# Performance work log

Hardware: AMD Instinct MI355X
Metric: run time of the kernel (lower is better)

The kernel has to match this reference:

```python
import jax, jax.numpy as jnp
import numpy as np
from jax import lax

N, L, D = 8, 2048, 512
KS = [3, 5]
DECAY = 0.2


def setup_inputs() -> dict:
    key = jax.random.key(0)
    k1, k2, k3, k4, k5 = jax.random.split(key, 5)
    return {
        "qa_embed_data": jax.random.normal(k1, (N, L, D), dtype=jnp.float32),
        "conv_w3": jax.random.normal(k2, (D, 1, KS[0]), dtype=jnp.float32) * (1.0 / KS[0]),
        "conv_w5": jax.random.normal(k3, (D, 1, KS[1]), dtype=jnp.float32) * (1.0 / KS[1]),
        "fusion_w": jax.random.normal(k4, (D, 2 * D), dtype=jnp.float32) * 0.02,
        "fusion_b": jax.random.normal(k5, (D,), dtype=jnp.float32) * 0.02,
    }


def causal_depthwise_conv(x, w, k):
    # x: [N, L, C], w: [C, 1, k] (depthwise, groups=C). Left-pad by k-1 (causal).
    xc = jnp.transpose(x, (0, 2, 1))  # [N, C, L]
    y = lax.conv_general_dilated(
        xc, w, window_strides=(1,), padding=[(k - 1, 0)],
        feature_group_count=x.shape[-1],
        dimension_numbers=("NCH", "OIH", "NCH"))
    return jnp.transpose(y, (0, 2, 1))  # [N, L, C]


def squash(v):
    norm = jnp.linalg.norm(v, axis=-1, keepdims=True)
    scale = norm ** 2 / (1.0 + norm ** 2)
    return scale * v / (norm + 1e-9)


def dynamic_routing(u, num_iterations):
    # u: [N, L, M, C]
    n, l, m, _ = u.shape
    logits = jnp.zeros((n, l, m), dtype=u.dtype)
    v = None
    for i in range(num_iterations):
        c = jax.nn.softmax(logits, axis=-1)
        s = jnp.einsum("nlm,nlmc->nlc", c, u)
        v = squash(s)
        if i < num_iterations - 1:
            logits = logits + jnp.einsum("nlmc,nlc->nlm", u, v)
    return v


def time_attention(x):
    # x: [N, L, C]; causal attention with exp(-decay*dist) bias -> add -decay*dist in log space
    l = x.shape[1]
    sim = jnp.einsum("nlc,nmc->nlm", x, x)  # [N, L, L]
    idx = jnp.arange(l)
    dist = (idx[:, None] - idx[None, :]).astype(x.dtype)  # query - key
    mask = dist >= 0  # lower-triangular causal mask
    ws = jnp.where(mask[None], sim - DECAY * dist[None], -jnp.inf)
    attn = jax.nn.softmax(ws, axis=-1)
    return jnp.einsum("nlm,nmc->nlc", attn, x)


def reference(qa_embed_data, conv_w3, conv_w5, fusion_w, fusion_b):
    trend3 = causal_depthwise_conv(qa_embed_data, conv_w3, KS[0])
    trend5 = causal_depthwise_conv(qa_embed_data, conv_w5, KS[1])
    seasonal = jnp.stack([qa_embed_data - trend3, qa_embed_data - trend5], axis=2)  # [N,L,2,C]
    trend = jnp.stack([trend3, trend5], axis=2)  # [N,L,2,C]
    seasonal_f = time_attention(dynamic_routing(seasonal, 3))
    trend_f = time_attention(dynamic_routing(trend, 3))
    cat = jnp.concatenate([seasonal_f, trend_f], axis=-1)  # [N,L,2C]
    return cat @ fusion_w.T + fusion_b
```

## Files before the change

### kernel.cpp

```cpp
#include <hip/hip_runtime.h>


typedef short     bf16x8 __attribute__((ext_vector_type(8)));
typedef float     f32x4  __attribute__((ext_vector_type(4)));
typedef unsigned short u16;
typedef u16       u16x8  __attribute__((ext_vector_type(8)));
typedef u16       u16x4  __attribute__((ext_vector_type(4)));

#define NBATCH 8
#define LSEQ   2048
#define DCH    512
#define DPAD   520
#define VSTR   40
#define DECAYF 0.2f
#define WTILES 4

typedef const __attribute__((address_space(1))) unsigned char* gas_t;
typedef __attribute__((address_space(3))) unsigned char* las_t;
__device__ __forceinline__ void dma16(const void* g, void* l) {
    __builtin_amdgcn_global_load_lds((gas_t)g, (las_t)l, 16, 0, 0);
}

__device__ __forceinline__ u16 f2bf(float f) {
    unsigned int u = __float_as_uint(f);
    u += 0x7fffu + ((u >> 16) & 1u);
    return (u16)(u >> 16);
}

__device__ __forceinline__ void wave_sum6(float& a, float& b, float& c,
                                          float& d, float& e, float& f) {
#pragma unroll
    for (int m = 1; m < 64; m <<= 1) {
        float ta = __shfl_xor(a, m, 64);
        float tb = __shfl_xor(b, m, 64);
        float tc = __shfl_xor(c, m, 64);
        float td = __shfl_xor(d, m, 64);
        float te = __shfl_xor(e, m, 64);
        float tf = __shfl_xor(f, m, 64);
        a += ta; b += tb; c += tc; d += td; e += te; f += tf;
    }
}

__global__ __launch_bounds__(256) void conv_route(
    const float* __restrict__ x, const float* __restrict__ w3, const float* __restrict__ w5,
    u16* __restrict__ vs, u16* __restrict__ vt)
{
    const int wid  = threadIdx.x >> 6;
    const int lane = threadIdx.x & 63;
    const int pp   = wid >> 1;
    const int half = wid & 1;
    const int p = blockIdx.x * 2 + pp;
    const int n = p >> 11, l = p & (LSEQ - 1);
    const int c0 = half * 256 + lane * 4;

    float xm[5][4];
#pragma unroll
    for (int j = 0; j < 5; ++j) {
        int ll = l - j;
        if (ll >= 0) {
            float4 a = *(const float4*)(x + ((size_t)(n*LSEQ + ll))*DCH + c0);
            xm[j][0]=a.x; xm[j][1]=a.y; xm[j][2]=a.z; xm[j][3]=a.w;
        } else {
#pragma unroll
            for (int i = 0; i < 4; ++i) xm[j][i] = 0.f;
        }
    }
    float f3[12], f5[20];
#pragma unroll
    for (int k = 0; k < 3; ++k) ((float4*)f3)[k] = ((const float4*)(w3 + (size_t)c0*3))[k];
#pragma unroll
    for (int k = 0; k < 5; ++k) ((float4*)f5)[k] = ((const float4*)(w5 + (size_t)c0*5))[k];

    float t3[4], t5[4], a0[4], a1[4];
#pragma unroll
    for (int i = 0; i < 4; ++i) {
        t3[i] = f3[i*3+0]*xm[2][i] + f3[i*3+1]*xm[1][i] + f3[i*3+2]*xm[0][i];
        t5[i] = f5[i*5+0]*xm[4][i] + f5[i*5+1]*xm[3][i] + f5[i*5+2]*xm[2][i]
              + f5[i*5+3]*xm[1][i] + f5[i*5+4]*xm[0][i];
        a0[i] = xm[0][i] - t3[i];
        a1[i] = xm[0][i] - t5[i];
    }

    float A1=0.f, B1=0.f, C1=0.f, A2=0.f, B2=0.f, C2=0.f;
#pragma unroll
    for (int i = 0; i < 4; ++i) {
        A1 += a0[i]*a0[i]; B1 += a0[i]*a1[i]; C1 += a1[i]*a1[i];
        A2 += t3[i]*t3[i]; B2 += t3[i]*t5[i]; C2 += t5[i]*t5[i];
    }
    wave_sum6(A1, B1, C1, A2, B2, C2);

    __shared__ float red[2][2][6];
    if (lane == 0) {
        red[pp][half][0] = A1; red[pp][half][1] = B1; red[pp][half][2] = C1;
        red[pp][half][3] = A2; red[pp][half][4] = B2; red[pp][half][5] = C2;
    }
    __syncthreads();
    A1 = red[pp][0][0] + red[pp][1][0];
    B1 = red[pp][0][1] + red[pp][1][1];
    C1 = red[pp][0][2] + red[pp][1][2];
    A2 = red[pp][0][3] + red[pp][1][3];
    B2 = red[pp][0][4] + red[pp][1][4];
    C2 = red[pp][0][5] + red[pp][1][5];

    float ba0=0.f, ba1=0.f, bb0=0.f, bb1=0.f;
    float ca0=0.5f, ca1=0.5f, sca=0.f, cb0=0.5f, cb1=0.5f, scb=0.f;
#pragma unroll
    for (int it = 0; it < 3; ++it) {
        float mxa = fmaxf(ba0, ba1), mxb = fmaxf(bb0, bb1);
        float ea0 = __expf(ba0-mxa), ea1 = __expf(ba1-mxa);
        float eb0 = __expf(bb0-mxb), eb1 = __expf(bb1-mxb);
        float ia = 1.f/(ea0+ea1), ib = 1.f/(eb0+eb1);
        ca0 = ea0*ia; ca1 = ea1*ia; cb0 = eb0*ib; cb1 = eb1*ib;
        float na = ca0*ca0*A1 + 2.f*ca0*ca1*B1 + ca1*ca1*C1;
        float nb = cb0*cb0*A2 + 2.f*cb0*cb1*B2 + cb1*cb1*C2;
        sca = na / ((1.f + na) * (sqrtf(na) + 1e-9f));
        scb = nb / ((1.f + nb) * (sqrtf(nb) + 1e-9f));
        if (it < 2) {
            ba0 += sca*(ca0*A1 + ca1*B1);
            ba1 += sca*(ca0*B1 + ca1*C1);
            bb0 += scb*(cb0*A2 + cb1*B2);
            bb1 += scb*(cb0*B2 + cb1*C2);
        }
    }
    u16x4 pa, pb;
#pragma unroll
    for (int i = 0; i < 4; ++i) {
        pa[i] = f2bf(sca*(ca0*a0[i] + ca1*a1[i]));
        pb[i] = f2bf(scb*(cb0*t3[i] + cb1*t5[i]));
    }
    *(u16x4*)(vs + (size_t)p*DPAD + c0) = pa;
    *(u16x4*)(vt + (size_t)p*DPAD + c0) = pb;
}

__global__ __launch_bounds__(256) void attn(
    const u16* __restrict__ vs, const u16* __restrict__ vt,
    u16* __restrict__ cat)
{
    __shared__ u16 Ks[33792/2];
    __shared__ u16 Vs[DCH*VSTR];
    __shared__ unsigned int Ps32[4][16][20];

    const int inst = blockIdx.y;
    const int t = inst >> 3, n = inst & 7;
    const u16* src = (t ? vt : vs) + (size_t)n * LSEQ * DPAD;

    const int bx = blockIdx.x;
    const int r0 = (((bx & 7) << 2) | (bx >> 3)) * 64;

    const int tid  = threadIdx.x;
    const int wid  = tid >> 6, lane = tid & 63;
    const int l16  = lane & 15, quad = lane >> 4;

    bf16x8 qf[16];
    {
        const u16* qp = src + (size_t)(r0 + wid*16 + l16) * DPAD + quad*8;
#pragma unroll
        for (int kc = 0; kc < 16; ++kc) qf[kc] = *(const bf16x8*)(qp + kc*32);
    }

    f32x4 O[32];
#pragma unroll
    for (int i = 0; i < 32; ++i) O[i] = (f32x4){0.f, 0.f, 0.f, 0.f};
    f32x4 O2 = {0.f, 0.f, 0.f, 0.f};

    bf16x8 ones8;
#pragma unroll
    for (int i = 0; i < 8; ++i) ones8[i] = (short)0x3F80;

    const int kb_hi = (r0 >> 5) + 1;
    const int kb_lo = (kb_hi >= WTILES) ? kb_hi - (WTILES-1) : 0;

    {
        const u16* gK = src + (size_t)kb_lo * 32 * DPAD;
        for (int i = wid; i < 33; i += 4) dma16(gK + i*512 + lane*8, Ks + i*512);
    }

    for (int kb = kb_lo; kb <= kb_hi; ++kb) {
        __syncthreads();

        f32x4 S0a = {0.f,0.f,0.f,0.f}, S1a = {0.f,0.f,0.f,0.f};
        f32x4 S0b = {0.f,0.f,0.f,0.f}, S1b = {0.f,0.f,0.f,0.f};
#pragma unroll
        for (int kc = 0; kc < 8; ++kc) {
            bf16x8 b0 = *(const bf16x8*)(Ks + (size_t)l16*DPAD + kc*32 + quad*8);
            bf16x8 b1 = *(const bf16x8*)(Ks + (size_t)(16+l16)*DPAD + kc*32 + quad*8);
            S0a = __builtin_amdgcn_mfma_f32_16x16x32_bf16(qf[kc], b0, S0a, 0, 0, 0);
            S1a = __builtin_amdgcn_mfma_f32_16x16x32_bf16(qf[kc], b1, S1a, 0, 0, 0);
        }
#pragma unroll
        for (int kc = 8; kc < 16; ++kc) {
            bf16x8 b0 = *(const bf16x8*)(Ks + (size_t)l16*DPAD + kc*32 + quad*8);
            bf16x8 b1 = *(const bf16x8*)(Ks + (size_t)(16+l16)*DPAD + kc*32 + quad*8);
            S0b = __builtin_amdgcn_mfma_f32_16x16x32_bf16(qf[kc], b0, S0b, 0, 0, 0);
            S1b = __builtin_amdgcn_mfma_f32_16x16x32_bf16(qf[kc], b1, S1b, 0, 0, 0);
        }
        f32x4 S0 = S0a + S0b, S1 = S1a + S1b;

#pragma unroll
        for (int pass = 0; pass < 2; ++pass) {
            const int ch = pass*256 + tid;
#pragma unroll
            for (int g = 0; g < 4; ++g) {
                u16x8 o;
#pragma unroll
                for (int j = 0; j < 4; ++j) {
                    o[2*j]   = Ks[(size_t)(g*4 + j)      * DPAD + ch];
                    o[2*j+1] = Ks[(size_t)(g*4 + j + 16) * DPAD + ch];
                }
                *(u16x8*)(Vs + ch*VSTR + g*8) = o;
            }
        }

        const int rowg = r0 + wid*16 + quad*4;
#pragma unroll
        for (int r = 0; r < 4; ++r) {
            int row = rowg + r;
            int d0  = row - (kb*32 + l16);
            int d1  = d0 - 16;
            float p0 = (d0 >= 0) ? __expf(fmaf(-DECAYF, (float)d0, S0[r] - 1.f)) : 0.f;
            float p1 = (d1 >= 0) ? __expf(fmaf(-DECAYF, (float)d1, S1[r] - 1.f)) : 0.f;
            Ps32[wid][quad*4 + r][l16] = ((unsigned)f2bf(p1) << 16) | (unsigned)f2bf(p0);
        }

        __syncthreads();
        if (kb < kb_hi) {
            const u16* gK = src + (size_t)(kb+1) * 32 * DPAD;
            for (int i = wid; i < 33; i += 4) dma16(gK + i*512 + lane*8, Ks + i*512);
        }

        bf16x8 pf = *(const bf16x8*)(&Ps32[wid][l16][quad*4]);
#pragma unroll
        for (int ct = 0; ct < 32; ++ct) {
            bf16x8 vf = *(const bf16x8*)(Vs + (size_t)(ct*16 + l16)*VSTR + quad*8);
            O[ct] = __builtin_amdgcn_mfma_f32_16x16x32_bf16(pf, vf, O[ct], 0, 0, 0);
        }
        O2 = __builtin_amdgcn_mfma_f32_16x16x32_bf16(pf, ones8, O2, 0, 0, 0);
    }

    float inv[4];
#pragma unroll
    for (int r = 0; r < 4; ++r) inv[r] = 1.f / O2[r];
    const size_t rowbase = (size_t)n * LSEQ + r0 + wid*16 + quad*4;
    const int colbase = t * 512 + l16;
#pragma unroll
    for (int ct = 0; ct < 32; ++ct) {
#pragma unroll
        for (int r = 0; r < 4; ++r)
            cat[(rowbase + r) * 1024 + colbase + ct*16] = f2bf(O[ct][r] * inv[r]);
    }
}

__global__ __launch_bounds__(256) void cast_w(const float* __restrict__ w, u16* __restrict__ wb)
{
    int id = blockIdx.x * 256 + threadIdx.x;
    float4 f = ((const float4*)w)[id];
    u16x4 o;
    o[0] = f2bf(f.x); o[1] = f2bf(f.y); o[2] = f2bf(f.z); o[3] = f2bf(f.w);
    ((u16x4*)wb)[id] = o;
}

__global__ __launch_bounds__(256) void fusion_gemm(
    const u16* __restrict__ A, const u16* __restrict__ Wb,
    const float* __restrict__ bias, float* __restrict__ out)
{
    __shared__ u16 As[2][64*64];
    __shared__ u16 Bs[2][128*64];
    const int m0 = blockIdx.x * 64;
    const int n0 = blockIdx.y * 128;
    const int tid = threadIdx.x;
    const int wid = tid >> 6, lane = tid & 63;
    const int l16 = lane & 15, quad = lane >> 4;

    f32x4 acc[4][2];
#pragma unroll
    for (int i = 0; i < 4; ++i)
#pragma unroll
        for (int j = 0; j < 2; ++j) acc[i][j] = (f32x4){0.f, 0.f, 0.f, 0.f};

    auto stage = [&](int kb_, int b_) {
#pragma unroll
        for (int i = 0; i < 2; ++i) {
            int q = i*256 + tid, r = q >> 3, kp = q & 7;
            int kl = kp ^ (r & 7);
            dma16(A + (size_t)(m0 + r)*1024 + kb_*64 + kl*8, As[b_] + q*8);
        }
#pragma unroll
        for (int i = 0; i < 4; ++i) {
            int q = i*256 + tid, r = q >> 3, kp = q & 7;
            int kl = kp ^ (r & 7);
            dma16(Wb + (size_t)(n0 + r)*1024 + kb_*64 + kl*8, Bs[b_] + q*8);
        }
    };

    stage(0, 0);
    for (int kb = 0; kb < 16; ++kb) {
        const int b = kb & 1;
        asm volatile("s_waitcnt vmcnt(0)" ::: "memory");
        __builtin_amdgcn_s_barrier();
        asm volatile("" ::: "memory");
        if (kb < 15) stage(kb + 1, b ^ 1);
#pragma unroll
        for (int k2 = 0; k2 < 2; ++k2) {
            const int kl = k2*4 + quad;
            bf16x8 af[4], bf2[2];
#pragma unroll
            for (int i = 0; i < 4; ++i) {
                int r = i*16 + l16;
                af[i] = *(const bf16x8*)(As[b] + r*64 + (kl ^ (r & 7))*8);
            }
#pragma unroll
            for (int j = 0; j < 2; ++j) {
                int r = wid*32 + j*16 + l16;
                bf2[j] = *(const bf16x8*)(Bs[b] + r*64 + (kl ^ (r & 7))*8);
            }
#pragma unroll
            for (int i = 0; i < 4; ++i)
#pragma unroll
                for (int j = 0; j < 2; ++j)
                    acc[i][j] = __builtin_amdgcn_mfma_f32_16x16x32_bf16(af[i], bf2[j], acc[i][j], 0, 0, 0);
        }
    }
#pragma unroll
    for (int j = 0; j < 2; ++j) {
        int col = n0 + wid*32 + j*16 + l16;
        float bv = bias[col];
#pragma unroll
        for (int i = 0; i < 4; ++i) {
            int rowb = m0 + i*16 + quad*4;
#pragma unroll
            for (int r = 0; r < 4; ++r)
                out[(size_t)(rowb + r)*512 + col] = acc[i][j][r] + bv;
        }
    }
}

extern "C" void kernel_launch(void* const* d_in, const int* in_sizes, int n_in,
                              void* d_out, int out_size, void* d_ws, size_t ws_size,
                              hipStream_t stream)
{
    (void)in_sizes; (void)n_in; (void)out_size; (void)ws_size;
    const float* x  = (const float*)d_in[0];
    const float* w3 = (const float*)d_in[1];
    const float* w5 = (const float*)d_in[2];
    const float* fw = (const float*)d_in[3];
    const float* fb = (const float*)d_in[4];
    float* out = (float*)d_out;

    const size_t SZP = (size_t)NBATCH * LSEQ * DPAD;
    u16* vs   = (u16*)d_ws;
    u16* vt   = vs   + SZP;
    u16* cat  = vt   + SZP;
    u16* wb   = cat  + (size_t)NBATCH*LSEQ*1024;

    cast_w     <<<512, 256, 0, stream>>>(fw, wb);
    conv_route <<<8192, 256, 0, stream>>>(x, w3, w5, vs, vt);
    attn       <<<dim3(32, 16), 256, 0, stream>>>(vs, vt, cat);
    fusion_gemm<<<dim3(256, 4), 256, 0, stream>>>(cat, wb, fb, out);
}
```

Before: 183.8 us.

## Double-buffer K tiles in attention and triple-buffer fusion GEMM loads

The attention kernel now keeps two K tile buffers in shared memory and prefetches two tiles ahead, waiting with vmcnt counters instead of a full __syncthreads, so global loads overlap the QK/PV compute. The V transpose loop reads 32-bit pairs and writes two channels per thread instead of separate 16-bit loads. The fusion GEMM moves from a double to a triple buffer with a prefetch distance of two. This raises LDS use per block, which may lower occupancy, and the padded extra DMA slots load redundant data.

Result: faster. 177.3 us (-3.5%).

```diff
diff --git a/kernel.cpp b/kernel.cpp
--- a/kernel.cpp
+++ b/kernel.cpp
@@ -6,6 +6,8 @@
 typedef unsigned short u16;
 typedef u16       u16x8  __attribute__((ext_vector_type(8)));
 typedef u16       u16x4  __attribute__((ext_vector_type(4)));
+typedef unsigned int u32;
+typedef u32       u32x4  __attribute__((ext_vector_type(4)));
 
 #define NBATCH 8
 #define LSEQ   2048
@@ -136,7 +138,7 @@
     const u16* __restrict__ vs, const u16* __restrict__ vt,
     u16* __restrict__ cat)
 {
-    __shared__ u16 Ks[33792/2];
+    __shared__ u16 KsB[2][18432];
     __shared__ u16 Vs[DCH*VSTR];
     __shared__ unsigned int Ps32[4][16][20];
 
@@ -170,44 +172,58 @@
     const int kb_hi = (r0 >> 5) + 1;
     const int kb_lo = (kb_hi >= WTILES) ? kb_hi - (WTILES-1) : 0;
 
-    {
-        const u16* gK = src + (size_t)kb_lo * 32 * DPAD;
-        for (int i = wid; i < 33; i += 4) dma16(gK + i*512 + lane*8, Ks + i*512);
-    }
+    auto stageK = [&](int kbt, int buf) {
+        const u16* gK = src + (size_t)kbt * 32 * DPAD;
+#pragma unroll
+        for (int j = 0; j < 9; ++j) {
+            int i = wid + 4*j;
+            int is = (i < 33) ? i : 0;
+            dma16(gK + is*512 + lane*8, KsB[buf] + i*512);
+        }
+    };
+
+    stageK(kb_lo,     0);
+    stageK(kb_lo + 1, 1);
 
     for (int kb = kb_lo; kb <= kb_hi; ++kb) {
-        __syncthreads();
+        if (kb < kb_hi) asm volatile("s_waitcnt vmcnt(9)" ::: "memory");
+        else            asm volatile("s_waitcnt vmcnt(0)" ::: "memory");
+        __builtin_amdgcn_s_barrier();
+        asm volatile("" ::: "memory");
+        const u16* K = KsB[(kb - kb_lo) & 1];
 
         f32x4 S0a = {0.f,0.f,0.f,0.f}, S1a = {0.f,0.f,0.f,0.f};
         f32x4 S0b = {0.f,0.f,0.f,0.f}, S1b = {0.f,0.f,0.f,0.f};
 #pragma unroll
         for (int kc = 0; kc < 8; ++kc) {
-            bf16x8 b0 = *(const bf16x8*)(Ks + (size_t)l16*DPAD + kc*32 + quad*8);
-            bf16x8 b1 = *(const bf16x8*)(Ks + (size_t)(16+l16)*DPAD + kc*32 + quad*8);
+            bf16x8 b0 = *(const bf16x8*)(K + (size_t)l16*DPAD + kc*32 + quad*8);
+            bf16x8 b1 = *(const bf16x8*)(K + (size_t)(16+l16)*DPAD + kc*32 + quad*8);
             S0a = __builtin_amdgcn_mfma_f32_16x16x32_bf16(qf[kc], b0, S0a, 0, 0, 0);
             S1a = __builtin_amdgcn_mfma_f32_16x16x32_bf16(qf[kc], b1, S1a, 0, 0, 0);
         }
 #pragma unroll
         for (int kc = 8; kc < 16; ++kc) {
-            bf16x8 b0 = *(const bf16x8*)(Ks + (size_t)l16*DPAD + kc*32 + quad*8);
-            bf16x8 b1 = *(const bf16x8*)(Ks + (size_t)(16+l16)*DPAD + kc*32 + quad*8);
+            bf16x8 b0 = *(const bf16x8*)(K + (size_t)l16*DPAD + kc*32 + quad*8);
+            bf16x8 b1 = *(const bf16x8*)(K + (size_t)(16+l16)*DPAD + kc*32 + quad*8);
             S0b = __builtin_amdgcn_mfma_f32_16x16x32_bf16(qf[kc], b0, S0b, 0, 0, 0);
             S1b = __builtin_amdgcn_mfma_f32_16x16x32_bf16(qf[kc], b1, S1b, 0, 0, 0);
         }
         f32x4 S0 = S0a + S0b, S1 = S1a + S1b;
 
-#pragma unroll
-        for (int pass = 0; pass < 2; ++pass) {
-            const int ch = pass*256 + tid;
+        {
+            const int ch2 = tid * 2;
 #pragma unroll
             for (int g = 0; g < 4; ++g) {
-                u16x8 o;
+                u32 pe[4], po[4];
 #pragma unroll
                 for (int j = 0; j < 4; ++j) {
-                    o[2*j]   = Ks[(size_t)(g*4 + j)      * DPAD + ch];
-                    o[2*j+1] = Ks[(size_t)(g*4 + j + 16) * DPAD + ch];
+                    u32 lo = *(const u32*)(K + (size_t)(g*4 + j)      * DPAD + ch2);
+                    u32 hi = *(const u32*)(K + (size_t)(g*4 + j + 16) * DPAD + ch2);
+                    pe[j] = (lo & 0xffffu) | (hi << 16);
+                    po[j] = (lo >> 16)     | (hi & 0xffff0000u);
                 }
-                *(u16x8*)(Vs + ch*VSTR + g*8) = o;
+                *(u32x4*)(Vs + (size_t)ch2*VSTR + g*8)       = (u32x4){pe[0],pe[1],pe[2],pe[3]};
+                *(u32x4*)(Vs + (size_t)(ch2+1)*VSTR + g*8)   = (u32x4){po[0],po[1],po[2],po[3]};
             }
         }
 
@@ -222,11 +238,10 @@
             Ps32[wid][quad*4 + r][l16] = ((unsigned)f2bf(p1) << 16) | (unsigned)f2bf(p0);
         }
 
-        __syncthreads();
-        if (kb < kb_hi) {
-            const u16* gK = src + (size_t)(kb+1) * 32 * DPAD;
-            for (int i = wid; i < 33; i += 4) dma16(gK + i*512 + lane*8, Ks + i*512);
-        }
+        asm volatile("s_waitcnt lgkmcnt(0)" ::: "memory");
+        __builtin_amdgcn_s_barrier();
+        asm volatile("" ::: "memory");
+        if (kb + 2 <= kb_hi) stageK(kb + 2, (kb - kb_lo) & 1);
 
         bf16x8 pf = *(const bf16x8*)(&Ps32[wid][l16][quad*4]);
 #pragma unroll
@@ -263,8 +278,8 @@
     const u16* __restrict__ A, const u16* __restrict__ Wb,
     const float* __restrict__ bias, float* __restrict__ out)
 {
-    __shared__ u16 As[2][64*64];
-    __shared__ u16 Bs[2][128*64];
+    __shared__ u16 As[3][64*64];
+    __shared__ u16 Bs[3][128*64];
     const int m0 = blockIdx.x * 64;
     const int n0 = blockIdx.y * 128;
     const int tid = threadIdx.x;
@@ -293,12 +308,14 @@
     };
 
     stage(0, 0);
+    stage(1, 1);
     for (int kb = 0; kb < 16; ++kb) {
-        const int b = kb & 1;
-        asm volatile("s_waitcnt vmcnt(0)" ::: "memory");
+        const int b = kb % 3;
+        if (kb < 15) asm volatile("s_waitcnt vmcnt(6)" ::: "memory");
+        else         asm volatile("s_waitcnt vmcnt(0)" ::: "memory");
         __builtin_amdgcn_s_barrier();
         asm volatile("" ::: "memory");
-        if (kb < 15) stage(kb + 1, b ^ 1);
+        if (kb < 14) stage(kb + 2, (kb + 2) % 3);
 #pragma unroll
         for (int k2 = 0; k2 < 2; ++k2) {
             const int kl = k2*4 + quad;
```
